# Kernel tuning notes

Hardware: AMD Instinct MI355X
Metric: run time of the kernel (lower is better)

Reference implementation:

```python
import jax, jax.numpy as jnp
import numpy as np

B, H, S = 2, 16, 2048
CTX = 1024
VD = 288          # valence_dim
FFN = 512         # ffn_dim
EPSILON = 0.066
LN_EPS = 1e-5


def layer_norm(x, w, b):
    mu = jnp.mean(x, axis=-1, keepdims=True)
    var = jnp.var(x, axis=-1, keepdims=True)
    return (x - mu) * jax.lax.rsqrt(var + LN_EPS) * w + b


def setup_inputs() -> dict:
    key = jax.random.key(0)
    ks = jax.random.split(key, 12)

    def lin(k, fan_in, fan_out):
        # torch nn.Linear default init: U(-1/sqrt(fan_in), 1/sqrt(fan_in)); stored as [in, out]
        bound = 1.0 / np.sqrt(fan_in)
        k1, k2 = jax.random.split(k)
        W = jax.random.uniform(k1, (fan_in, fan_out), jnp.float32, -bound, bound)
        b = jax.random.uniform(k2, (fan_out,), jnp.float32, -bound, bound)
        return W, b

    attention_scores = jax.random.normal(ks[0], (B, H, S, S), jnp.float32)
    input_ids = jax.random.randint(ks[1], (B, S), 0, CTX)

    # xavier_uniform for embedding weight [CTX, VD]
    xb = np.sqrt(6.0 / (CTX + VD))
    emb_W = jax.random.uniform(ks[2], (CTX, VD), jnp.float32, -xb, xb)

    pW1, pb1 = lin(ks[3], VD, 2 * VD)
    pW2, pb2 = lin(ks[4], 2 * VD, H)
    fW1, fb1 = lin(ks[5], H + 1, FFN)
    fW2, fb2 = lin(ks[6], FFN, FFN // 2)
    fW3, fb3 = lin(ks[7], FFN // 2, 1)

    return {
        "attention_scores": attention_scores,
        "input_ids": input_ids,
        "emb_W": emb_W,
        "ln_v_w": jnp.ones((VD,), jnp.float32),
        "ln_v_b": jnp.zeros((VD,), jnp.float32),
        "pW1": pW1, "pb1": pb1, "pW2": pW2, "pb2": pb2,
        "ln_c_w": jnp.ones((H + 1,), jnp.float32),
        "ln_c_b": jnp.zeros((H + 1,), jnp.float32),
        "fW1": fW1, "fb1": fb1, "fW2": fW2, "fb2": fb2, "fW3": fW3, "fb3": fb3,
    }


def reference(attention_scores, input_ids, emb_W, ln_v_w, ln_v_b,
              pW1, pb1, pW2, pb2, ln_c_w, ln_c_b,
              fW1, fb1, fW2, fb2, fW3, fb3):
    # token_occurrence buffer starts at zero: new_occ = 0.87*0 + clamp(counts, 1)
    counts = jnp.bincount(input_ids.reshape(-1), length=CTX).astype(jnp.float32)
    counts = jnp.maximum(counts, 1.0)
    occ = jnp.log1p(counts[input_ids])                        # [B, S]

    v = layer_norm(emb_W[input_ids], ln_v_w, ln_v_b)           # [B, S, VD]
    h = jax.nn.gelu(v @ pW1 + pb1, approximate=False)          # [B, S, 2*VD]
    valence_scores = jnp.tanh(h @ pW2 + pb2)                   # [B, S, H]

    comb = jnp.concatenate([occ[..., None], valence_scores], axis=-1)  # [B, S, H+1]
    comb = layer_norm(comb, ln_c_w, ln_c_b)

    h2 = jax.nn.gelu(comb @ fW1 + fb1, approximate=False)      # [B, S, FFN]
    h3 = jax.nn.gelu(h2 @ fW2 + fb2, approximate=False)        # [B, S, FFN//2]
    mod = jnp.tanh(h3 @ fW3 + fb3)                             # [B, S, 1]

    retrieval_weights = 1.0 + EPSILON * mod[:, None, :, :]     # [B, 1, S, 1]
    return attention_scores * retrieval_weights
```

## Files before the change

### kernel.cpp

```cpp
#include <hip/hip_runtime.h>
#include <math.h>

#define B_ 2
#define H_ 16
#define S_ 2048
#define CTX_ 1024
#define VD_ 288
#define VD2_ 576
#define FFN_ 512
#define FFNH_ 256
#define NH1_ 17
#define EPSILON_ 0.066f
#define LN_EPS_ 1e-5f
#define TPB_ 8
#define NBLK_ (B_ * S_ / TPB_)

typedef float vfloat4 __attribute__((ext_vector_type(4)));

__device__ __forceinline__ float gelu_exact(float x) {
    return 0.5f * x * (1.0f + erff(x * 0.70710678118654752440f));
}
__device__ __forceinline__ vfloat4 gelu4(vfloat4 v) {
    vfloat4 o;
    o.x = gelu_exact(v.x); o.y = gelu_exact(v.y);
    o.z = gelu_exact(v.z); o.w = gelu_exact(v.w);
    return o;
}

__global__ __launch_bounds__(1024) void count_kernel(
    const int* __restrict__ ids, int* __restrict__ counts)
{
    __shared__ int hist[CTX_];
    const int t = threadIdx.x;
    hist[t] = 0;
    __syncthreads();
    #pragma unroll
    for (int r = 0; r < (B_ * S_) / 1024; ++r)
        atomicAdd(&hist[ids[t + 1024 * r]], 1);
    __syncthreads();
    counts[t] = hist[t];
}

__global__ __launch_bounds__(512, 4) void token_mlp_scale_kernel(
    const int* __restrict__ ids, const int* __restrict__ counts,
    const float* __restrict__ embW,
    const float* __restrict__ lnvw, const float* __restrict__ lnvb,
    const float* __restrict__ pW1, const float* __restrict__ pb1,
    const float* __restrict__ pW2, const float* __restrict__ pb2,
    const float* __restrict__ lncw, const float* __restrict__ lncb,
    const float* __restrict__ fW1, const float* __restrict__ fb1,
    const float* __restrict__ fW2, const float* __restrict__ fb2,
    const float* __restrict__ fW3, const float* __restrict__ fb3,
    const vfloat4* __restrict__ scores, vfloat4* __restrict__ out)
{
    __shared__ __align__(16) float va[VD_][TPB_];
    __shared__ __align__(16) float ha[VD2_][TPB_];
    __shared__ __align__(16) float comb17[NH1_][TPB_];
    __shared__ __align__(16) float h2a[FFN_][TPB_];
    __shared__ __align__(16) float h3a[FFNH_][TPB_];
    __shared__ float wl[TPB_];

    const int tid  = threadIdx.x;
    const int tok0 = blockIdx.x * TPB_;
    const int wid  = tid >> 6;
    const int cthr = tid & 63;
    const int quad = wid & 1;
    const int cq   = wid >> 1;
    const int tq   = quad * 4;

    {
        const int w  = wid;
        const int l  = cthr;
        const int id = ids[tok0 + w];
        float x[5];
        float s = 0.f, sq = 0.f;
        #pragma unroll
        for (int r = 0; r < 4; ++r) {
            float xv = embW[id * VD_ + l + 64 * r];
            x[r] = xv; s += xv; sq += xv * xv;
        }
        x[4] = 0.f;
        if (l < 32) {
            float xv = embW[id * VD_ + 256 + l];
            x[4] = xv; s += xv; sq += xv * xv;
        }
        #pragma unroll
        for (int m = 32; m >= 1; m >>= 1) {
            s  += __shfl_xor(s,  m, 64);
            sq += __shfl_xor(sq, m, 64);
        }
        float mu   = s * (1.f / VD_);
        float var  = sq * (1.f / VD_) - mu * mu;
        float rstd = rsqrtf(var + LN_EPS_);
        #pragma unroll
        for (int r = 0; r < 4; ++r) {
            int i = l + 64 * r;
            va[i][w] = (x[r] - mu) * rstd * lnvw[i] + lnvb[i];
        }
        if (l < 32) {
            int i = 256 + l;
            va[i][w] = (x[4] - mu) * rstd * lnvw[i] + lnvb[i];
        }
    }
    __syncthreads();

    {
        vfloat4 a0 = 0, a1 = 0, a2 = 0;
        const int cb = 144 * cq;
        const bool extra = (cthr < 16);
        for (int k = 0; k < VD_; k += 8) {
            float w0[8], w1[8], w2[8];
            #pragma unroll
            for (int u = 0; u < 8; ++u) {
                const float* wr = &pW1[(k + u) * VD2_ + cb + cthr];
                w0[u] = wr[0]; w1[u] = wr[64];
                if (extra) w2[u] = wr[128];
            }
            vfloat4 v[8];
            #pragma unroll
            for (int u = 0; u < 8; ++u) v[u] = *(const vfloat4*)&va[k + u][tq];
            #pragma unroll
            for (int u = 0; u < 8; ++u) {
                a0 += w0[u] * v[u];
                a1 += w1[u] * v[u];
                if (extra) a2 += w2[u] * v[u];
            }
        }
        int col = cb + cthr;
        *(vfloat4*)&ha[col     ][tq] = gelu4(a0 + pb1[col]);
        *(vfloat4*)&ha[col + 64][tq] = gelu4(a1 + pb1[col + 64]);
        if (extra)
            *(vfloat4*)&ha[col + 128][tq] = gelu4(a2 + pb1[col + 128]);
    }
    __syncthreads();

    if (wid < 4) {
        const int t0  = wid * 2;
        const int col = cthr & 15;
        const int ks  = cthr >> 4;
        float2 acc = make_float2(0.f, 0.f);
        for (int k = ks * 144; k < ks * 144 + 144; k += 8) {
            float w[8]; float2 v[8];
            #pragma unroll
            for (int u = 0; u < 8; ++u) w[u] = pW2[(k + u) * H_ + col];
            #pragma unroll
            for (int u = 0; u < 8; ++u) v[u] = *(const float2*)&ha[k + u][t0];
            #pragma unroll
            for (int u = 0; u < 8; ++u) {
                acc.x += w[u] * v[u].x; acc.y += w[u] * v[u].y;
            }
        }
        acc.x += __shfl_xor(acc.x, 16, 64); acc.y += __shfl_xor(acc.y, 16, 64);
        acc.x += __shfl_xor(acc.x, 32, 64); acc.y += __shfl_xor(acc.y, 32, 64);
        if (cthr < 16) {
            float b = pb2[col];
            float2 o = make_float2(tanhf(acc.x + b), tanhf(acc.y + b));
            *(float2*)&comb17[1 + col][t0] = o;
        }
        if (cthr == 16) {
            #pragma unroll
            for (int j = 0; j < 2; ++j) {
                int t = t0 + j;
                int id = ids[tok0 + t];
                float c = (float)counts[id];
                if (c < 1.f) c = 1.f;
                comb17[0][t] = log1pf(c);
            }
        }
    }
    __syncthreads();

    if (tid < TPB_) {
        float vals[NH1_];
        float s = 0.f;
        #pragma unroll
        for (int i = 0; i < NH1_; ++i) { vals[i] = comb17[i][tid]; s += vals[i]; }
        float mu = s / NH1_;
        float vq = 0.f;
        #pragma unroll
        for (int i = 0; i < NH1_; ++i) { float d = vals[i] - mu; vq += d * d; }
        float r = rsqrtf(vq / NH1_ + LN_EPS_);
        #pragma unroll
        for (int i = 0; i < NH1_; ++i)
            comb17[i][tid] = (vals[i] - mu) * r * lncw[i] + lncb[i];
    }
    __syncthreads();

    {
        vfloat4 a0 = 0, a1 = 0;
        const int cb = 128 * cq;
        #pragma unroll
        for (int k = 0; k < NH1_; ++k) {
            vfloat4 v = *(const vfloat4*)&comb17[k][tq];
            const float* wr = &fW1[k * FFN_ + cb + cthr];
            a0 += wr[0] * v;
            a1 += wr[64] * v;
        }
        int col = cb + cthr;
        *(vfloat4*)&h2a[col     ][tq] = gelu4(a0 + fb1[col]);
        *(vfloat4*)&h2a[col + 64][tq] = gelu4(a1 + fb1[col + 64]);
    }
    __syncthreads();

    {
        vfloat4 a0 = 0;
        const int cb = 64 * cq;
        for (int k = 0; k < FFN_; k += 8) {
            float w0[8]; vfloat4 v[8];
            #pragma unroll
            for (int u = 0; u < 8; ++u)
                w0[u] = fW2[(k + u) * FFNH_ + cb + cthr];
            #pragma unroll
            for (int u = 0; u < 8; ++u) v[u] = *(const vfloat4*)&h2a[k + u][tq];
            #pragma unroll
            for (int u = 0; u < 8; ++u) a0 += w0[u] * v[u];
        }
        int col = cb + cthr;
        *(vfloat4*)&h3a[col][tq] = gelu4(a0 + fb2[col]);
    }
    __syncthreads();

    {
        const int tt = wid;
        const int l  = cthr;
        float acc = 0.f;
        #pragma unroll
        for (int r = 0; r < FFNH_ / 64; ++r) {
            int k = l + 64 * r;
            acc += h3a[k][tt] * fW3[k];
        }
        #pragma unroll
        for (int m = 32; m >= 1; m >>= 1) acc += __shfl_xor(acc, m, 64);
        if (l == 0)
            wl[tt] = 1.0f + EPSILON_ * tanhf(acc + fb3[0]);
    }
    __syncthreads();

    {
        const int g0 = blockIdx.x * TPB_;
        #pragma unroll 4
        for (int m = tid; m < TPB_ * H_ * (S_ / 4); m += 512) {
            int rr  = m >> 9;
            int off = m & 511;
            int j   = rr & 7;
            int h   = rr >> 3;
            int g   = g0 + j;
            long row = (long)(g >> 11) * (H_ * S_) + h * S_ + (g & (S_ - 1));
            long idx = row * (S_ / 4) + off;
            vfloat4 x = __builtin_nontemporal_load(&scores[idx]);
            x *= wl[j];
            __builtin_nontemporal_store(x, &out[idx]);
        }
    }
}

extern "C" void kernel_launch(void* const* d_in, const int* in_sizes, int n_in,
                              void* d_out, int out_size, void* d_ws, size_t ws_size,
                              hipStream_t stream) {
    const float* scores = (const float*)d_in[0];
    const int*   ids    = (const int*)  d_in[1];
    const float* embW   = (const float*)d_in[2];
    const float* lnvw   = (const float*)d_in[3];
    const float* lnvb   = (const float*)d_in[4];
    const float* pW1    = (const float*)d_in[5];
    const float* pb1    = (const float*)d_in[6];
    const float* pW2    = (const float*)d_in[7];
    const float* pb2    = (const float*)d_in[8];
    const float* lncw   = (const float*)d_in[9];
    const float* lncb   = (const float*)d_in[10];
    const float* fW1    = (const float*)d_in[11];
    const float* fb1    = (const float*)d_in[12];
    const float* fW2    = (const float*)d_in[13];
    const float* fb2    = (const float*)d_in[14];
    const float* fW3    = (const float*)d_in[15];
    const float* fb3    = (const float*)d_in[16];

    int* counts = (int*)d_ws;

    count_kernel<<<1, 1024, 0, stream>>>(ids, counts);
    token_mlp_scale_kernel<<<NBLK_, 512, 0, stream>>>(
        ids, counts, embW, lnvw, lnvb, pW1, pb1, pW2, pb2,
        lncw, lncb, fW1, fb1, fW2, fb2, fW3, fb3,
        (const vfloat4*)scores, (vfloat4*)d_out);
}
```

Before: 249.2 us.

## Repartition MLP matmuls so each thread covers all tokens; split-K fW2

The first projection (pW1) is remapped so each thread computes one or two output columns across all 8 tokens of the block, instead of several columns for 4 tokens. Each weight load from global memory is now reused across twice as many tokens, and the unroll depth goes to 16. The fW2 layer uses a split-K across the two halves of the warps, reducing partial sums through shared memory reused from the va buffer with an extra barrier. This aims to halve global weight traffic per FLOP, at the cost of more registers and a serialized reduction step.

```diff
diff --git a/kernel.cpp b/kernel.cpp
--- a/kernel.cpp
+++ b/kernel.cpp
@@ -105,32 +105,34 @@
     __syncthreads();
 
     {
-        vfloat4 a0 = 0, a1 = 0, a2 = 0;
-        const int cb = 144 * cq;
-        const bool extra = (cthr < 16);
-        for (int k = 0; k < VD_; k += 8) {
-            float w0[8], w1[8], w2[8];
-            #pragma unroll
-            for (int u = 0; u < 8; ++u) {
+        const int cb = 72 * wid;
+        const bool extra = (cthr < 8);
+        vfloat4 a0l = 0, a0h = 0, a1l = 0, a1h = 0;
+        for (int k = 0; k < VD_; k += 16) {
+            float w0[16], w1[16];
+            #pragma unroll
+            for (int u = 0; u < 16; ++u) {
                 const float* wr = &pW1[(k + u) * VD2_ + cb + cthr];
-                w0[u] = wr[0]; w1[u] = wr[64];
-                if (extra) w2[u] = wr[128];
-            }
-            vfloat4 v[8];
-            #pragma unroll
-            for (int u = 0; u < 8; ++u) v[u] = *(const vfloat4*)&va[k + u][tq];
-            #pragma unroll
-            for (int u = 0; u < 8; ++u) {
-                a0 += w0[u] * v[u];
-                a1 += w1[u] * v[u];
-                if (extra) a2 += w2[u] * v[u];
+                w0[u] = wr[0];
+                if (extra) w1[u] = wr[64];
+            }
+            #pragma unroll
+            for (int u = 0; u < 16; ++u) {
+                vfloat4 vl = *(const vfloat4*)&va[k + u][0];
+                vfloat4 vh = *(const vfloat4*)&va[k + u][4];
+                a0l += w0[u] * vl; a0h += w0[u] * vh;
+                if (extra) { a1l += w1[u] * vl; a1h += w1[u] * vh; }
             }
         }
         int col = cb + cthr;
-        *(vfloat4*)&ha[col     ][tq] = gelu4(a0 + pb1[col]);
-        *(vfloat4*)&ha[col + 64][tq] = gelu4(a1 + pb1[col + 64]);
-        if (extra)
-            *(vfloat4*)&ha[col + 128][tq] = gelu4(a2 + pb1[col + 128]);
+        float b0 = pb1[col];
+        *(vfloat4*)&ha[col][0] = gelu4(a0l + b0);
+        *(vfloat4*)&ha[col][4] = gelu4(a0h + b0);
+        if (extra) {
+            float b1 = pb1[col + 64];
+            *(vfloat4*)&ha[col + 64][0] = gelu4(a1l + b1);
+            *(vfloat4*)&ha[col + 64][4] = gelu4(a1h + b1);
+        }
     }
     __syncthreads();
 
@@ -203,20 +205,37 @@
     __syncthreads();
 
     {
-        vfloat4 a0 = 0;
-        const int cb = 64 * cq;
-        for (int k = 0; k < FFN_; k += 8) {
-            float w0[8]; vfloat4 v[8];
-            #pragma unroll
-            for (int u = 0; u < 8; ++u)
+        float* part = (float*)va;
+        const int cs = wid & 3;
+        const int kh = wid >> 2;
+        const int cb = 64 * cs;
+        const int k0 = kh * 256;
+        vfloat4 a0l = 0, a0h = 0;
+        for (int k = k0; k < k0 + 256; k += 16) {
+            float w0[16];
+            #pragma unroll
+            for (int u = 0; u < 16; ++u)
                 w0[u] = fW2[(k + u) * FFNH_ + cb + cthr];
             #pragma unroll
-            for (int u = 0; u < 8; ++u) v[u] = *(const vfloat4*)&h2a[k + u][tq];
-            #pragma unroll
-            for (int u = 0; u < 8; ++u) a0 += w0[u] * v[u];
-        }
-        int col = cb + cthr;
-        *(vfloat4*)&h3a[col][tq] = gelu4(a0 + fb2[col]);
+            for (int u = 0; u < 16; ++u) {
+                vfloat4 vl = *(const vfloat4*)&h2a[k + u][0];
+                vfloat4 vh = *(const vfloat4*)&h2a[k + u][4];
+                a0l += w0[u] * vl; a0h += w0[u] * vh;
+            }
+        }
+        const int col = cb + cthr;
+        if (kh) {
+            *(vfloat4*)&part[col * 8 + 0] = a0l;
+            *(vfloat4*)&part[col * 8 + 4] = a0h;
+        }
+        __syncthreads();
+        if (!kh) {
+            vfloat4 pl = *(const vfloat4*)&part[col * 8 + 0];
+            vfloat4 ph = *(const vfloat4*)&part[col * 8 + 4];
+            float b = fb2[col];
+            *(vfloat4*)&h3a[col][0] = gelu4(a0l + pl + b);
+            *(vfloat4*)&h3a[col][4] = gelu4(a0h + ph + b);
+        }
     }
     __syncthreads();
 
```

After: 258.4 us. +3.7%, slower.

## Add producer wavefront that prefetches scores into cache during token MLP

Applied to the files above, without the earlier changes.

Adds a ninth wavefront per block that, during each MLP stage, issues loads of the first half of this block's attention-score rows into cache so the later scaling pass hits cache instead of HBM. The prefetched region is then read with normal loads and the rest with nontemporal loads, and the scaling loop strides over 576 threads. The aim is to overlap the memory-bound stream with the compute-bound per-token MLP. In exchange the block is larger, with possible occupancy loss, extra cache pressure, and a risk that prefetched lines are evicted before reuse.

```diff
diff --git a/kernel.cpp b/kernel.cpp
--- a/kernel.cpp
+++ b/kernel.cpp
@@ -14,6 +14,7 @@
 #define LN_EPS_ 1e-5f
 #define TPB_ 8
 #define NBLK_ (B_ * S_ / TPB_)
+#define NTHR_ 576
 
 typedef float vfloat4 __attribute__((ext_vector_type(4)));
 
@@ -41,7 +42,7 @@
     counts[t] = hist[t];
 }
 
-__global__ __launch_bounds__(512, 4) void token_mlp_scale_kernel(
+__global__ __launch_bounds__(NTHR_, 4) void token_mlp_scale_kernel(
     const int* __restrict__ ids, const int* __restrict__ counts,
     const float* __restrict__ embW,
     const float* __restrict__ lnvw, const float* __restrict__ lnvb,
@@ -68,7 +69,32 @@
     const int cq   = wid >> 1;
     const int tq   = quad * 4;
 
-    {
+    float pacc = 0.f;
+    int   pm   = 0;
+    const int g0 = blockIdx.x * TPB_;
+    auto prefetch = [&](int n) {
+        for (int i = 0; i < n; i += 8) {
+            vfloat4 x[8];
+            #pragma unroll
+            for (int u = 0; u < 8; ++u) {
+                int m   = (pm + i + u) * 64 + cthr;
+                int rr  = m >> 9;
+                int off = m & 511;
+                int j   = rr & 7;
+                int h   = rr >> 3;
+                int gt  = g0 + j;
+                long row = (long)(gt >> 11) * (H_ * S_) + h * S_ + (gt & (S_ - 1));
+                x[u] = scores[row * (S_ / 4) + off];
+            }
+            #pragma unroll
+            for (int u = 0; u < 8; ++u) pacc += x[u].x;
+        }
+        pm += n;
+    };
+
+    if (wid == 8) {
+        prefetch(32);
+    } else {
         const int w  = wid;
         const int l  = cthr;
         const int id = ids[tok0 + w];
@@ -104,7 +130,9 @@
     }
     __syncthreads();
 
-    {
+    if (wid == 8) {
+        prefetch(160);
+    } else {
         vfloat4 a0 = 0, a1 = 0, a2 = 0;
         const int cb = 144 * cq;
         const bool extra = (cthr < 16);
@@ -134,7 +162,9 @@
     }
     __syncthreads();
 
-    if (wid < 4) {
+    if (wid == 8) {
+        prefetch(96);
+    } else if (wid < 4) {
         const int t0  = wid * 2;
         const int col = cthr & 15;
         const int ks  = cthr >> 4;
@@ -170,6 +200,7 @@
     }
     __syncthreads();
 
+    if (wid == 8) prefetch(16);
     if (tid < TPB_) {
         float vals[NH1_];
         float s = 0.f;
@@ -186,7 +217,9 @@
     }
     __syncthreads();
 
-    {
+    if (wid == 8) {
+        prefetch(48);
+    } else {
         vfloat4 a0 = 0, a1 = 0;
         const int cb = 128 * cq;
         #pragma unroll
@@ -202,7 +235,9 @@
     }
     __syncthreads();
 
-    {
+    if (wid == 8) {
+        prefetch(160);
+    } else {
         vfloat4 a0 = 0;
         const int cb = 64 * cq;
         for (int k = 0; k < FFN_; k += 8) {
@@ -220,7 +255,7 @@
     }
     __syncthreads();
 
-    {
+    if (wid < 8) {
         const int tt = wid;
         const int l  = cthr;
         float acc = 0.f;
@@ -236,10 +271,11 @@
     }
     __syncthreads();
 
+    asm volatile("" :: "v"(pacc));
+
     {
-        const int g0 = blockIdx.x * TPB_;
         #pragma unroll 4
-        for (int m = tid; m < TPB_ * H_ * (S_ / 4); m += 512) {
+        for (int m = tid; m < TPB_ * H_ * (S_ / 4); m += NTHR_) {
             int rr  = m >> 9;
             int off = m & 511;
             int j   = rr & 7;
@@ -247,7 +283,8 @@
             int g   = g0 + j;
             long row = (long)(g >> 11) * (H_ * S_) + h * S_ + (g & (S_ - 1));
             long idx = row * (S_ / 4) + off;
-            vfloat4 x = __builtin_nontemporal_load(&scores[idx]);
+            vfloat4 x = (m < 32768) ? scores[idx]
+                                    : __builtin_nontemporal_load(&scores[idx]);
             x *= wl[j];
             __builtin_nontemporal_store(x, &out[idx]);
         }
@@ -278,7 +315,7 @@
     int* counts = (int*)d_ws;
 
     count_kernel<<<1, 1024, 0, stream>>>(ids, counts);
-    token_mlp_scale_kernel<<<NBLK_, 512, 0, stream>>>(
+    token_mlp_scale_kernel<<<NBLK_, NTHR_, 0, stream>>>(
         ids, counts, embW, lnvw, lnvb, pW1, pb1, pW2, pb2,
         lncw, lncb, fW1, fb1, fW2, fb2, fW3, fb3,
         (const vfloat4*)scores, (vfloat4*)d_out);
```

Result: slower. 344.6 us (+38.2%).
